# Performance work log

Measured on AMD Instinct MI355X. Metric: run time of the kernel, lower is better.

## Reference

```python
import jax, jax.numpy as jnp
import numpy as np

B, C, H, W = 8, 384, 32, 32
NH, DK, DV = 8, 48, 48
CFF = 4 * C
L = H * W
NBIAS = (2 * H - 1) * (2 * W - 1)
LN_EPS = 1e-5


def _relative_indices(height, width):
    # rel_idx[q, k] = (gy_k - gy_q + H) * W + (gx_k - gx_q + W), matching the torch loop
    gy, gx = np.meshgrid(np.arange(height), np.arange(width), indexing='ij')
    gy = gy.ravel(); gx = gx.ravel()
    rel = (gy[None, :] - gy[:, None] + height) * width + (gx[None, :] - gx[:, None] + width)
    return jnp.asarray(rel, dtype=jnp.int64)


def setup_inputs() -> dict:
    key = jax.random.key(0)
    ks = jax.random.split(key, 10)
    s = 0.02  # small init scale
    return {
        'x': jax.random.normal(ks[0], (B, C, H, W), dtype=jnp.float32),
        'gamma': jnp.ones((C,), jnp.float32),
        'beta': jnp.zeros((C,), jnp.float32),
        'Wq': jax.random.normal(ks[1], (NH * DK, C), jnp.float32) * s,
        'Wk': jax.random.normal(ks[2], (NH * DK, C), jnp.float32) * s,
        'Wv': jax.random.normal(ks[3], (NH * DV, C), jnp.float32) * s,
        'Wo': jax.random.normal(ks[4], (C, NH * DV), jnp.float32) * s,
        'bo': jnp.zeros((C,), jnp.float32),
        'rel_bias': jax.random.normal(ks[5], (NH, NBIAS), jnp.float32),
        'fc1_w': jax.random.normal(ks[6], (CFF, C), jnp.float32) * s,
        'fc1_b': jnp.zeros((CFF,), jnp.float32),
        'fc2_w': jax.random.normal(ks[7], (C, CFF), jnp.float32) * s,
        'fc2_b': jnp.zeros((C,), jnp.float32),
        'rel_idx': _relative_indices(H, W),
    }


def reference(x, gamma, beta, Wq, Wk, Wv, Wo, bo, rel_bias,
              fc1_w, fc1_b, fc2_w, fc2_b, rel_idx):
    b, c, h_sp, w_sp = x.shape
    l = h_sp * w_sp
    nh = rel_bias.shape[0]
    dk = Wq.shape[0] // nh
    dv = Wv.shape[0] // nh

    # LayerNorm over channel dim (NHWC), then flatten to tokens [b, l, c]
    t = jnp.transpose(x, (0, 2, 3, 1))
    mu = jnp.mean(t, axis=-1, keepdims=True)
    var = jnp.mean(jnp.square(t - mu), axis=-1, keepdims=True)
    t = (t - mu) / jnp.sqrt(var + LN_EPS) * gamma + beta
    tok = t.reshape(b, l, c)

    q = (tok @ Wq.T).reshape(b, l, nh, dk)
    k = (tok @ Wk.T).reshape(b, l, nh, dk)
    v = (tok @ Wv.T).reshape(b, l, nh, dv)

    # gathered relative position bias: [nh, l, l]
    bias = rel_bias[:, rel_idx]
    # note: original applies NO 1/sqrt(d_k) scaling
    scores = jnp.einsum('blhd,bmhd->bhlm', q, k) + bias[None]
    attn = jax.nn.softmax(scores, axis=-1)
    out = jnp.einsum('bhlm,bmhd->blhd', attn, v).reshape(b, l, nh * dv)
    out = out @ Wo.T + bo  # [b, l, c]
    out = jnp.transpose(out, (0, 2, 1)).reshape(b, c, h_sp, w_sp)

    y = x + out  # attention residual (x_stem = x, no downsampling)

    # FFN: 1x1 convs == per-pixel linear over channels; exact (erf) gelu as torch default
    u = jnp.einsum('bchw,oc->bohw', y, fc1_w) + fc1_b[None, :, None, None]
    u = jax.nn.gelu(u, approximate=False)
    u = jnp.einsum('bchw,oc->bohw', u, fc2_w) + fc2_b[None, :, None, None]
    return y + u
```

## Files before the change

### kernel.cpp

```cpp
#include <hip/hip_runtime.h>
#include <math.h>

#define SL 1024
#define CH 384
#define NHEAD 8
#define DH 48
#define NBIAS 3969
#define NTOK 8192
#define BATCH 8
#define CFF 1536
#define LN_EPS 1e-5f
#define QKVLD 1152

#define WQKV_OFF 0
#define WO_OFF   442368
#define F1_OFF   589824
#define F2_OFF   1179648
#define WTOT     1769472

typedef float floatx4 __attribute__((ext_vector_type(4)));
typedef short bf16x8 __attribute__((ext_vector_type(8)));

__device__ __forceinline__ unsigned f2bf_u(float f) {
  unsigned u = __float_as_uint(f);
  return (u + 0x7fffu + ((u >> 16) & 1u)) >> 16;
}
__device__ __forceinline__ unsigned pack2(float a, float b) {
  return f2bf_u(a) | (f2bf_u(b) << 16);
}

__device__ __forceinline__ void gload_lds16(const void* g, void* l) {
  __builtin_amdgcn_global_load_lds(
      (const __attribute__((address_space(1))) void*)g,
      (__attribute__((address_space(3))) void*)l, 16, 0, 0);
}

__global__ void k_transpose_in(const float* __restrict__ x, float* __restrict__ xt) {
  __shared__ float s[32][33];
  int b = blockIdx.z;
  int c0 = blockIdx.y * 32, l0 = blockIdx.x * 32;
  int tx = threadIdx.x, ty = threadIdx.y;
  const float* xb = x + (size_t)b * CH * SL;
  float* xtb = xt + (size_t)b * SL * CH;
#pragma unroll
  for (int i = 0; i < 4; i++) {
    int c = c0 + ty * 4 + i;
    s[ty * 4 + i][tx] = xb[(size_t)c * SL + l0 + tx];
  }
  __syncthreads();
#pragma unroll
  for (int i = 0; i < 4; i++) {
    int l = l0 + ty * 4 + i;
    xtb[(size_t)l * CH + c0 + tx] = s[tx][ty * 4 + i];
  }
}

__global__ void k_transpose_add_out(const float* __restrict__ y, const float* __restrict__ u,
                                    float* __restrict__ out) {
  __shared__ float s[32][33];
  int b = blockIdx.z;
  int c0 = blockIdx.y * 32, l0 = blockIdx.x * 32;
  int tx = threadIdx.x, ty = threadIdx.y;
  const float* yb = y + (size_t)b * SL * CH;
  const float* ub = u + (size_t)b * SL * CH;
  float* ob = out + (size_t)b * CH * SL;
#pragma unroll
  for (int i = 0; i < 4; i++) {
    int l = l0 + ty * 4 + i;
    size_t idx = (size_t)l * CH + c0 + tx;
    s[ty * 4 + i][tx] = yb[idx] + ub[idx];
  }
  __syncthreads();
#pragma unroll
  for (int i = 0; i < 4; i++) {
    int c = c0 + ty * 4 + i;
    ob[(size_t)c * SL + l0 + tx] = s[tx][ty * 4 + i];
  }
}

__global__ void k_w2bf(const float* __restrict__ Wq, const float* __restrict__ Wk,
                       const float* __restrict__ Wv, const float* __restrict__ Wo,
                       const float* __restrict__ f1, const float* __restrict__ f2,
                       short* __restrict__ dst) {
  size_t i = ((size_t)blockIdx.x * 256 + threadIdx.x) * 8;
  if (i >= WTOT) return;
  const float* s;
  size_t base;
  if (i < 147456)        { s = Wq; base = 0; }
  else if (i < 294912)   { s = Wk; base = 147456; }
  else if (i < WO_OFF)   { s = Wv; base = 294912; }
  else if (i < F1_OFF)   { s = Wo; base = WO_OFF; }
  else if (i < F2_OFF)   { s = f1; base = F1_OFF; }
  else                   { s = f2; base = F2_OFF; }
  const float4* p = (const float4*)(s + (i - base));
  float4 a = p[0], b = p[1];
  uint4 o;
  o.x = pack2(a.x, a.y); o.y = pack2(a.z, a.w);
  o.z = pack2(b.x, b.y); o.w = pack2(b.z, b.w);
  *(uint4*)(dst + i) = o;
}

__global__ void k_layernorm(const float* __restrict__ xt, const float* __restrict__ gamma,
                            const float* __restrict__ beta, short* __restrict__ tok) {
  int t = blockIdx.x;
  const float* row = xt + (size_t)t * CH;
  short* orow = tok + (size_t)t * CH;
  int tid = threadIdx.x;
  float v0 = row[tid], v1 = row[tid + 128], v2 = row[tid + 256];
  float s = v0 + v1 + v2;
  float q = v0 * v0 + v1 * v1 + v2 * v2;
#pragma unroll
  for (int mask = 32; mask; mask >>= 1) {
    s += __shfl_xor(s, mask, 64);
    q += __shfl_xor(q, mask, 64);
  }
  __shared__ float sh[4];
  if ((tid & 63) == 0) {
    sh[(tid >> 6) * 2] = s;
    sh[(tid >> 6) * 2 + 1] = q;
  }
  __syncthreads();
  s = sh[0] + sh[2];
  q = sh[1] + sh[3];
  float mu = s * (1.0f / CH);
  float var = q * (1.0f / CH) - mu * mu;
  float rstd = rsqrtf(var + LN_EPS);
  orow[tid]       = (short)f2bf_u((v0 - mu) * rstd * gamma[tid] + beta[tid]);
  orow[tid + 128] = (short)f2bf_u((v1 - mu) * rstd * gamma[tid + 128] + beta[tid + 128]);
  orow[tid + 256] = (short)f2bf_u((v2 - mu) * rstd * gamma[tid + 256] + beta[tid + 256]);
}

template <int BM, bool GELU, bool HAS_BIAS, bool HAS_RES, bool OUT_F32, bool OUT_BF>
__global__ __launch_bounds__(256) void k_gemm_mfma(
    const short* __restrict__ A, const short* __restrict__ W,
    const float* __restrict__ bias, const float* __restrict__ res,
    float* __restrict__ Cf, short* __restrict__ Cb, int N, int K) {
  constexpr int MI = BM / 32;
  constexpr int ASI = BM * 2 / 64;
  __shared__ short As[BM * 64];
  __shared__ short Bs[128 * 64];
  int tid = threadIdx.x;
  int wid = tid >> 6, lane = tid & 63;
  int lanelo = lane & 15, quad = lane >> 4;
  int wm = wid & 1, wn = wid >> 1;
  int m0 = blockIdx.y * BM, n0 = blockIdx.x * 128;

  const short* Aga[ASI];
  short* Ala[ASI];
#pragma unroll
  for (int s = 0; s < ASI; s++) {
    int p = wid * (BM * 2) + s * 64 + lane;
    int row = p >> 3, ch = (p & 7) ^ (row & 7);
    Aga[s] = A + (size_t)(m0 + row) * K + ch * 8;
    Ala[s] = As + (wid * (BM * 2) + s * 64) * 8;
  }
  const short* Bga[4];
  short* Bla[4];
#pragma unroll
  for (int s = 0; s < 4; s++) {
    int p = wid * 256 + s * 64 + lane;
    int row = p >> 3, ch = (p & 7) ^ (row & 7);
    Bga[s] = W + (size_t)(n0 + row) * K + ch * 8;
    Bla[s] = Bs + (wid * 256 + s * 64) * 8;
  }

  floatx4 acc[MI][4];
#pragma unroll
  for (int i = 0; i < MI; i++)
#pragma unroll
    for (int j = 0; j < 4; j++) acc[i][j] = {0.f, 0.f, 0.f, 0.f};

  int x8 = lanelo & 7;
  int ca0 = (quad ^ x8) * 8;
  int ca1 = ((quad + 4) ^ x8) * 8;

  for (int k0 = 0; k0 < K; k0 += 64) {
    __syncthreads();
#pragma unroll
    for (int s = 0; s < ASI; s++) gload_lds16(Aga[s] + k0, Ala[s]);
#pragma unroll
    for (int s = 0; s < 4; s++) gload_lds16(Bga[s] + k0, Bla[s]);
    __syncthreads();
#pragma unroll
    for (int h = 0; h < 2; h++) {
      int co = h ? ca1 : ca0;
      bf16x8 af[MI], bq[4];
#pragma unroll
      for (int i = 0; i < MI; i++)
        af[i] = *(const bf16x8*)&As[(wm * (BM / 2) + i * 16 + lanelo) * 64 + co];
#pragma unroll
      for (int j = 0; j < 4; j++)
        bq[j] = *(const bf16x8*)&Bs[(wn * 64 + j * 16 + lanelo) * 64 + co];
#pragma unroll
      for (int i = 0; i < MI; i++)
#pragma unroll
        for (int j = 0; j < 4; j++)
          acc[i][j] = __builtin_amdgcn_mfma_f32_16x16x32_bf16(af[i], bq[j], acc[i][j], 0, 0, 0);
    }
  }

  int colb = n0 + wn * 64 + lanelo;
  float bvv[4];
#pragma unroll
  for (int j = 0; j < 4; j++) bvv[j] = HAS_BIAS ? bias[colb + j * 16] : 0.0f;
#pragma unroll
  for (int i = 0; i < MI; i++) {
    int r = m0 + wm * (BM / 2) + i * 16 + quad * 4;
#pragma unroll
    for (int j = 0; j < 4; j++) {
      int c = colb + j * 16;
#pragma unroll
      for (int reg = 0; reg < 4; reg++) {
        float v = acc[i][j][reg] + bvv[j];
        size_t idx = (size_t)(r + reg) * N + c;
        if (HAS_RES) v += res[idx];
        if (GELU) v = 0.5f * v * (1.0f + erff(v * 0.7071067811865476f));
        if (OUT_F32) Cf[idx] = v;
        if (OUT_BF) Cb[idx] = (short)f2bf_u(v);
      }
    }
  }
}

__global__ __launch_bounds__(256) void k_attn_mfma(
    const short* __restrict__ qkv, const float* __restrict__ rel_bias,
    short* __restrict__ ao) {
  __shared__ short Qs[64 * 72];
  __shared__ short Ks[64 * 72];
  __shared__ short Vts[48 * 72];
  __shared__ short Ps[4 * 16 * 72];

  int b = blockIdx.z, h = blockIdx.y;
  int l0 = blockIdx.x * 64;
  int tid = threadIdx.x;
  int wid = tid >> 6, lane = tid & 63;
  int lanelo = lane & 15, quad = lane >> 4;
  size_t bSL = (size_t)b * SL;
  const float* rbh = rel_bias + h * NBIAS;

  int srow = tid / 3, spos = tid - srow * 3;
  int vmp = tid & 31, vdg = tid >> 5;

  if (tid < 192) {
    const short* src = qkv + (bSL + l0 + srow) * QKVLD + h * DH;
    *(uint4*)&Qs[srow * 72 + spos * 8]      = *(const uint4*)(src + spos * 8);
    *(uint4*)&Qs[srow * 72 + 24 + spos * 8] = *(const uint4*)(src + 24 + spos * 8);
  }
  for (int z = tid; z < 64 * 8; z += 256) {
    int r = z >> 3, u = z & 7;
    ((unsigned*)&Qs[r * 72 + 48])[u] = 0u;
    ((unsigned*)&Ks[r * 72 + 48])[u] = 0u;
  }
  __syncthreads();

  bf16x8 aq0 = *(const bf16x8*)&Qs[(wid * 16 + lanelo) * 72 + quad * 8];
  bf16x8 aq1 = *(const bf16x8*)&Qs[(wid * 16 + lanelo) * 72 + 32 + quad * 8];

  floatx4 O0 = {0.f, 0.f, 0.f, 0.f}, O1 = O0, O2 = O0;
  float lsum[4] = {0.f, 0.f, 0.f, 0.f};

  const float* rb[4];
  {
    int lq = l0 + wid * 16 + quad * 4;
#pragma unroll
    for (int reg = 0; reg < 4; reg++) {
      int l = lq + reg;
      rb[reg] = rbh + (1056 - (l >> 5) * 32 - (l & 31)) + lanelo;
    }
  }

  short* Pw = &Ps[wid * 16 * 72];

  for (int mt = 0; mt < SL; mt += 64) {
    __syncthreads();
    if (tid < 192) {
      {
        const short* src = qkv + (bSL + mt + srow) * QKVLD + 384 + h * DH;
        *(uint4*)&Ks[srow * 72 + spos * 8]      = *(const uint4*)(src + spos * 8);
        *(uint4*)&Ks[srow * 72 + 24 + spos * 8] = *(const uint4*)(src + 24 + spos * 8);
      }
      {
        const short* vs0 = qkv + (bSL + mt + 2 * vmp) * QKVLD + 768 + h * DH + vdg * 8;
        union { uint4 u; unsigned short s[8]; } va, vb;
        va.u = *(const uint4*)vs0;
        vb.u = *(const uint4*)(vs0 + QKVLD);
#pragma unroll
        for (int i = 0; i < 8; i++) {
          unsigned pk = (unsigned)va.s[i] | ((unsigned)vb.s[i] << 16);
          *(unsigned*)&Vts[(vdg * 8 + i) * 72 + 2 * vmp] = pk;
        }
      }
    }
    __syncthreads();

    floatx4 sarr[4];
#pragma unroll
    for (int nt = 0; nt < 4; nt++) {
      floatx4 acc = {0.f, 0.f, 0.f, 0.f};
      bf16x8 b0 = *(const bf16x8*)&Ks[(nt * 16 + lanelo) * 72 + quad * 8];
      bf16x8 b1 = *(const bf16x8*)&Ks[(nt * 16 + lanelo) * 72 + 32 + quad * 8];
      acc = __builtin_amdgcn_mfma_f32_16x16x32_bf16(aq0, b0, acc, 0, 0, 0);
      acc = __builtin_amdgcn_mfma_f32_16x16x32_bf16(aq1, b1, acc, 0, 0, 0);
      sarr[nt] = acc;
    }

#pragma unroll
    for (int nt = 0; nt < 4; nt++) {
      int mo = mt + nt * 16;
#pragma unroll
      for (int reg = 0; reg < 4; reg++) {
        float e = __expf(sarr[nt][reg] + rb[reg][mo]);
        lsum[reg] += e;
        Pw[(quad * 4 + reg) * 72 + nt * 16 + lanelo] = (short)f2bf_u(e);
      }
    }
    __asm__ volatile("s_waitcnt lgkmcnt(0)" ::: "memory");
    bf16x8 pa0 = *(const bf16x8*)&Pw[lanelo * 72 + quad * 8];
    bf16x8 pa1 = *(const bf16x8*)&Pw[lanelo * 72 + 32 + quad * 8];

    {
      bf16x8 vb0 = *(const bf16x8*)&Vts[(0 * 16 + lanelo) * 72 + quad * 8];
      bf16x8 vb1 = *(const bf16x8*)&Vts[(0 * 16 + lanelo) * 72 + 32 + quad * 8];
      O0 = __builtin_amdgcn_mfma_f32_16x16x32_bf16(pa0, vb0, O0, 0, 0, 0);
      O0 = __builtin_amdgcn_mfma_f32_16x16x32_bf16(pa1, vb1, O0, 0, 0, 0);
    }
    {
      bf16x8 vb0 = *(const bf16x8*)&Vts[(1 * 16 + lanelo) * 72 + quad * 8];
      bf16x8 vb1 = *(const bf16x8*)&Vts[(1 * 16 + lanelo) * 72 + 32 + quad * 8];
      O1 = __builtin_amdgcn_mfma_f32_16x16x32_bf16(pa0, vb0, O1, 0, 0, 0);
      O1 = __builtin_amdgcn_mfma_f32_16x16x32_bf16(pa1, vb1, O1, 0, 0, 0);
    }
    {
      bf16x8 vb0 = *(const bf16x8*)&Vts[(2 * 16 + lanelo) * 72 + quad * 8];
      bf16x8 vb1 = *(const bf16x8*)&Vts[(2 * 16 + lanelo) * 72 + 32 + quad * 8];
      O2 = __builtin_amdgcn_mfma_f32_16x16x32_bf16(pa0, vb0, O2, 0, 0, 0);
      O2 = __builtin_amdgcn_mfma_f32_16x16x32_bf16(pa1, vb1, O2, 0, 0, 0);
    }
  }

#pragma unroll
  for (int reg = 0; reg < 4; reg++) {
    float s = lsum[reg];
    s += __shfl_xor(s, 1, 64);
    s += __shfl_xor(s, 2, 64);
    s += __shfl_xor(s, 4, 64);
    s += __shfl_xor(s, 8, 64);
    float inv = 1.0f / s;
    size_t base = (bSL + (size_t)(l0 + wid * 16 + quad * 4 + reg)) * CH + h * DH;
    ao[base + 0 + lanelo]  = (short)f2bf_u(O0[reg] * inv);
    ao[base + 16 + lanelo] = (short)f2bf_u(O1[reg] * inv);
    ao[base + 32 + lanelo] = (short)f2bf_u(O2[reg] * inv);
  }
}

extern "C" void kernel_launch(void* const* d_in, const int* in_sizes, int n_in,
                              void* d_out, int out_size, void* d_ws, size_t ws_size,
                              hipStream_t stream) {
  const float* x = (const float*)d_in[0];
  const float* gamma = (const float*)d_in[1];
  const float* beta = (const float*)d_in[2];
  const float* Wq = (const float*)d_in[3];
  const float* Wk = (const float*)d_in[4];
  const float* Wv = (const float*)d_in[5];
  const float* Wo = (const float*)d_in[6];
  const float* bo = (const float*)d_in[7];
  const float* rel_bias = (const float*)d_in[8];
  const float* fc1_w = (const float*)d_in[9];
  const float* fc1_b = (const float*)d_in[10];
  const float* fc2_w = (const float*)d_in[11];
  const float* fc2_b = (const float*)d_in[12];
  float* out = (float*)d_out;

  const size_t TOKCH = (size_t)NTOK * CH;
  float* ws_f = (float*)d_ws;
  float* xt = ws_f;
  float* yb = xt + TOKCH;
  float* ub = yb + TOKCH;
  short* sbase = (short*)(ub + TOKCH);
  short* wbf    = sbase;
  short* tok_bf = wbf + WTOT;
  short* qkv_bf = tok_bf + TOKCH;
  short* ao_bf  = qkv_bf + (size_t)NTOK * QKVLD;
  short* yb_bf  = ao_bf + TOKCH;
  short* h1_bf  = yb_bf + TOKCH;

  dim3 tgrid(SL / 32, CH / 32, BATCH);
  dim3 tblk(32, 8);
  k_transpose_in<<<tgrid, tblk, 0, stream>>>(x, xt);
  k_w2bf<<<WTOT / 8 / 256, 256, 0, stream>>>(Wq, Wk, Wv, Wo, fc1_w, fc2_w, wbf);
  k_layernorm<<<NTOK, 128, 0, stream>>>(xt, gamma, beta, tok_bf);

  k_gemm_mfma<128, false, false, false, false, true>
      <<<dim3(QKVLD / 128, NTOK / 128), 256, 0, stream>>>(
          tok_bf, wbf + WQKV_OFF, nullptr, nullptr, nullptr, qkv_bf, QKVLD, CH);

  k_attn_mfma<<<dim3(SL / 64, NHEAD, BATCH), 256, 0, stream>>>(qkv_bf, rel_bias, ao_bf);

  k_gemm_mfma<64, false, true, true, true, true>
      <<<dim3(CH / 128, NTOK / 64), 256, 0, stream>>>(
          ao_bf, wbf + WO_OFF, bo, xt, yb, yb_bf, CH, CH);

  k_gemm_mfma<128, true, true, false, false, true>
      <<<dim3(CFF / 128, NTOK / 128), 256, 0, stream>>>(
          yb_bf, wbf + F1_OFF, fc1_b, nullptr, nullptr, h1_bf, CFF, CH);

  k_gemm_mfma<64, false, true, false, true, false>
      <<<dim3(CH / 128, NTOK / 64), 256, 0, stream>>>(
          h1_bf, wbf + F2_OFF, fc2_b, nullptr, ub, nullptr, CH, CFF);

  k_transpose_add_out<<<tgrid, tblk, 0, stream>>>(yb, ub, out);
}
```

Measured before the change: 229.5 us.

## Fuse input/output transposes into LayerNorm and GEMM epilogues; widen attention tile

The input NCHW-to-token transpose is folded into a new LayerNorm kernel that stages a 32-token by 384-channel tile in LDS. The Wo GEMM now reads its residual straight from NCHW x, and the fc2 GEMM adds the yb residual and writes NCHW output directly, which removes two transpose kernels and the xt and ub intermediates. Attention now handles 128 query rows per block with two 16-row sub-tiles per wave, reusing each K/V LDS load for twice as many rows, and the P buffer shares space with Q. The trade-offs are strided float4 stores of the output in the GEMM epilogue and higher register and LDS use per block in attention and LayerNorm.

```diff
diff --git a/kernel.cpp b/kernel.cpp
--- a/kernel.cpp
+++ b/kernel.cpp
@@ -33,49 +33,6 @@
   __builtin_amdgcn_global_load_lds(
       (const __attribute__((address_space(1))) void*)g,
       (__attribute__((address_space(3))) void*)l, 16, 0, 0);
-}
-
-__global__ void k_transpose_in(const float* __restrict__ x, float* __restrict__ xt) {
-  __shared__ float s[32][33];
-  int b = blockIdx.z;
-  int c0 = blockIdx.y * 32, l0 = blockIdx.x * 32;
-  int tx = threadIdx.x, ty = threadIdx.y;
-  const float* xb = x + (size_t)b * CH * SL;
-  float* xtb = xt + (size_t)b * SL * CH;
-#pragma unroll
-  for (int i = 0; i < 4; i++) {
-    int c = c0 + ty * 4 + i;
-    s[ty * 4 + i][tx] = xb[(size_t)c * SL + l0 + tx];
-  }
-  __syncthreads();
-#pragma unroll
-  for (int i = 0; i < 4; i++) {
-    int l = l0 + ty * 4 + i;
-    xtb[(size_t)l * CH + c0 + tx] = s[tx][ty * 4 + i];
-  }
-}
-
-__global__ void k_transpose_add_out(const float* __restrict__ y, const float* __restrict__ u,
-                                    float* __restrict__ out) {
-  __shared__ float s[32][33];
-  int b = blockIdx.z;
-  int c0 = blockIdx.y * 32, l0 = blockIdx.x * 32;
-  int tx = threadIdx.x, ty = threadIdx.y;
-  const float* yb = y + (size_t)b * SL * CH;
-  const float* ub = u + (size_t)b * SL * CH;
-  float* ob = out + (size_t)b * CH * SL;
-#pragma unroll
-  for (int i = 0; i < 4; i++) {
-    int l = l0 + ty * 4 + i;
-    size_t idx = (size_t)l * CH + c0 + tx;
-    s[ty * 4 + i][tx] = yb[idx] + ub[idx];
-  }
-  __syncthreads();
-#pragma unroll
-  for (int i = 0; i < 4; i++) {
-    int c = c0 + ty * 4 + i;
-    ob[(size_t)c * SL + l0 + tx] = s[tx][ty * 4 + i];
-  }
 }
 
 __global__ void k_w2bf(const float* __restrict__ Wq, const float* __restrict__ Wk,
@@ -100,41 +57,50 @@
   *(uint4*)(dst + i) = o;
 }
 
-__global__ void k_layernorm(const float* __restrict__ xt, const float* __restrict__ gamma,
-                            const float* __restrict__ beta, short* __restrict__ tok) {
-  int t = blockIdx.x;
-  const float* row = xt + (size_t)t * CH;
-  short* orow = tok + (size_t)t * CH;
+__global__ __launch_bounds__(256) void k_ln_fused(
+    const float* __restrict__ x, const float* __restrict__ gamma,
+    const float* __restrict__ beta, short* __restrict__ tok) {
+  __shared__ float sx[32][385];
+  int b = blockIdx.y, l0 = blockIdx.x * 32;
   int tid = threadIdx.x;
-  float v0 = row[tid], v1 = row[tid + 128], v2 = row[tid + 256];
-  float s = v0 + v1 + v2;
-  float q = v0 * v0 + v1 * v1 + v2 * v2;
-#pragma unroll
-  for (int mask = 32; mask; mask >>= 1) {
-    s += __shfl_xor(s, mask, 64);
-    q += __shfl_xor(q, mask, 64);
-  }
-  __shared__ float sh[4];
-  if ((tid & 63) == 0) {
-    sh[(tid >> 6) * 2] = s;
-    sh[(tid >> 6) * 2 + 1] = q;
+  const float* xb = x + (size_t)b * CH * SL;
+  int cr = tid >> 3, ls = (tid & 7) * 4;
+#pragma unroll
+  for (int c0 = 0; c0 < CH; c0 += 32) {
+    int c = c0 + cr;
+    float4 v = *(const float4*)(xb + (size_t)c * SL + l0 + ls);
+    sx[ls + 0][c] = v.x; sx[ls + 1][c] = v.y;
+    sx[ls + 2][c] = v.z; sx[ls + 3][c] = v.w;
   }
   __syncthreads();
-  s = sh[0] + sh[2];
-  q = sh[1] + sh[3];
+  int tl = tid >> 3, p = tid & 7;
+  float vals[48];
+  float s = 0.f, q = 0.f;
+#pragma unroll
+  for (int i = 0; i < 48; i++) {
+    float v = sx[tl][p * 48 + i];
+    vals[i] = v; s += v; q += v * v;
+  }
+  s += __shfl_xor(s, 1, 64); q += __shfl_xor(q, 1, 64);
+  s += __shfl_xor(s, 2, 64); q += __shfl_xor(q, 2, 64);
+  s += __shfl_xor(s, 4, 64); q += __shfl_xor(q, 4, 64);
   float mu = s * (1.0f / CH);
-  float var = q * (1.0f / CH) - mu * mu;
-  float rstd = rsqrtf(var + LN_EPS);
-  orow[tid]       = (short)f2bf_u((v0 - mu) * rstd * gamma[tid] + beta[tid]);
-  orow[tid + 128] = (short)f2bf_u((v1 - mu) * rstd * gamma[tid + 128] + beta[tid + 128]);
-  orow[tid + 256] = (short)f2bf_u((v2 - mu) * rstd * gamma[tid + 256] + beta[tid + 256]);
-}
-
-template <int BM, bool GELU, bool HAS_BIAS, bool HAS_RES, bool OUT_F32, bool OUT_BF>
+  float rstd = rsqrtf(q * (1.0f / CH) - mu * mu + LN_EPS);
+  short* orow = tok + (size_t)(b * SL + l0 + tl) * CH + p * 48;
+#pragma unroll
+  for (int i = 0; i < 48; i += 2) {
+    float a = (vals[i] - mu) * rstd * gamma[p * 48 + i] + beta[p * 48 + i];
+    float c = (vals[i + 1] - mu) * rstd * gamma[p * 48 + i + 1] + beta[p * 48 + i + 1];
+    *(unsigned*)(orow + i) = pack2(a, c);
+  }
+}
+
+template <int BM, bool GELU, bool HAS_BIAS, int RES_MODE, int OUT_MODE>
 __global__ __launch_bounds__(256) void k_gemm_mfma(
     const short* __restrict__ A, const short* __restrict__ W,
     const float* __restrict__ bias, const float* __restrict__ res,
-    float* __restrict__ Cf, short* __restrict__ Cb, int N, int K) {
+    float* __restrict__ Cf, short* __restrict__ Cb, float* __restrict__ Ct,
+    int N, int K) {
   constexpr int MI = BM / 32;
   constexpr int ASI = BM * 2 / 64;
   __shared__ short As[BM * 64];
@@ -206,17 +172,32 @@
 #pragma unroll
   for (int i = 0; i < MI; i++) {
     int r = m0 + wm * (BM / 2) + i * 16 + quad * 4;
+    int bb = r >> 10, ll = r & 1023;
 #pragma unroll
     for (int j = 0; j < 4; j++) {
       int c = colb + j * 16;
+      float4 rv = {0.f, 0.f, 0.f, 0.f};
+      if (RES_MODE == 2) rv = *(const float4*)(res + ((size_t)bb * CH + c) * SL + ll);
+      float vv[4];
 #pragma unroll
       for (int reg = 0; reg < 4; reg++) {
         float v = acc[i][j][reg] + bvv[j];
-        size_t idx = (size_t)(r + reg) * N + c;
-        if (HAS_RES) v += res[idx];
+        if (RES_MODE == 1) v += res[(size_t)(r + reg) * N + c];
+        if (RES_MODE == 2) v += (&rv.x)[reg];
         if (GELU) v = 0.5f * v * (1.0f + erff(v * 0.7071067811865476f));
-        if (OUT_F32) Cf[idx] = v;
-        if (OUT_BF) Cb[idx] = (short)f2bf_u(v);
+        vv[reg] = v;
+      }
+      if (OUT_MODE & 1) {
+#pragma unroll
+        for (int reg = 0; reg < 4; reg++) Cf[(size_t)(r + reg) * N + c] = vv[reg];
+      }
+      if (OUT_MODE & 2) {
+#pragma unroll
+        for (int reg = 0; reg < 4; reg++) Cb[(size_t)(r + reg) * N + c] = (short)f2bf_u(vv[reg]);
+      }
+      if (OUT_MODE & 4) {
+        float4 ov = {vv[0], vv[1], vv[2], vv[3]};
+        *(float4*)(Ct + ((size_t)bb * CH + c) * SL + ll) = ov;
       }
     }
   }
@@ -225,13 +206,12 @@
 __global__ __launch_bounds__(256) void k_attn_mfma(
     const short* __restrict__ qkv, const float* __restrict__ rel_bias,
     short* __restrict__ ao) {
-  __shared__ short Qs[64 * 72];
+  __shared__ short QP[128 * 72];
   __shared__ short Ks[64 * 72];
   __shared__ short Vts[48 * 72];
-  __shared__ short Ps[4 * 16 * 72];
 
   int b = blockIdx.z, h = blockIdx.y;
-  int l0 = blockIdx.x * 64;
+  int l0 = blockIdx.x * 128;
   int tid = threadIdx.x;
   int wid = tid >> 6, lane = tid & 63;
   int lanelo = lane & 15, quad = lane >> 4;
@@ -241,35 +221,37 @@
   int srow = tid / 3, spos = tid - srow * 3;
   int vmp = tid & 31, vdg = tid >> 5;
 
-  if (tid < 192) {
-    const short* src = qkv + (bSL + l0 + srow) * QKVLD + h * DH;
-    *(uint4*)&Qs[srow * 72 + spos * 8]      = *(const uint4*)(src + spos * 8);
-    *(uint4*)&Qs[srow * 72 + 24 + spos * 8] = *(const uint4*)(src + 24 + spos * 8);
-  }
-  for (int z = tid; z < 64 * 8; z += 256) {
+  for (int g = tid; g < 768; g += 256) {
+    int row = g / 6, pos = g - row * 6;
+    *(uint4*)&QP[row * 72 + pos * 8] =
+        *(const uint4*)(qkv + (bSL + l0 + row) * QKVLD + h * DH + pos * 8);
+  }
+  for (int z = tid; z < 128 * 8; z += 256) {
     int r = z >> 3, u = z & 7;
-    ((unsigned*)&Qs[r * 72 + 48])[u] = 0u;
-    ((unsigned*)&Ks[r * 72 + 48])[u] = 0u;
+    ((unsigned*)&QP[r * 72 + 48])[u] = 0u;
+    if (r < 64) ((unsigned*)&Ks[r * 72 + 48])[u] = 0u;
   }
   __syncthreads();
 
-  bf16x8 aq0 = *(const bf16x8*)&Qs[(wid * 16 + lanelo) * 72 + quad * 8];
-  bf16x8 aq1 = *(const bf16x8*)&Qs[(wid * 16 + lanelo) * 72 + 32 + quad * 8];
-
-  floatx4 O0 = {0.f, 0.f, 0.f, 0.f}, O1 = O0, O2 = O0;
-  float lsum[4] = {0.f, 0.f, 0.f, 0.f};
-
-  const float* rb[4];
-  {
-    int lq = l0 + wid * 16 + quad * 4;
-#pragma unroll
-    for (int reg = 0; reg < 4; reg++) {
-      int l = lq + reg;
-      rb[reg] = rbh + (1056 - (l >> 5) * 32 - (l & 31)) + lanelo;
-    }
-  }
-
-  short* Pw = &Ps[wid * 16 * 72];
+  bf16x8 aq[2][2];
+#pragma unroll
+  for (int i = 0; i < 2; i++) {
+    aq[i][0] = *(const bf16x8*)&QP[(wid * 32 + i * 16 + lanelo) * 72 + quad * 8];
+    aq[i][1] = *(const bf16x8*)&QP[(wid * 32 + i * 16 + lanelo) * 72 + 32 + quad * 8];
+  }
+
+  floatx4 O[2][3];
+#pragma unroll
+  for (int i = 0; i < 2; i++)
+#pragma unroll
+    for (int d = 0; d < 3; d++) O[i][d] = {0.f, 0.f, 0.f, 0.f};
+  float lsum[2][4] = {{0.f, 0.f, 0.f, 0.f}, {0.f, 0.f, 0.f, 0.f}};
+  int boff[2];
+#pragma unroll
+  for (int i = 0; i < 2; i++)
+    boff[i] = 1056 - (l0 + wid * 32 + i * 16 + quad * 4) + lanelo;
+
+  short* Pw = &QP[wid * 32 * 72];
 
   for (int mt = 0; mt < SL; mt += 64) {
     __syncthreads();
@@ -293,64 +275,69 @@
     }
     __syncthreads();
 
-    floatx4 sarr[4];
+    bf16x8 kb[4][2];
 #pragma unroll
     for (int nt = 0; nt < 4; nt++) {
-      floatx4 acc = {0.f, 0.f, 0.f, 0.f};
-      bf16x8 b0 = *(const bf16x8*)&Ks[(nt * 16 + lanelo) * 72 + quad * 8];
-      bf16x8 b1 = *(const bf16x8*)&Ks[(nt * 16 + lanelo) * 72 + 32 + quad * 8];
-      acc = __builtin_amdgcn_mfma_f32_16x16x32_bf16(aq0, b0, acc, 0, 0, 0);
-      acc = __builtin_amdgcn_mfma_f32_16x16x32_bf16(aq1, b1, acc, 0, 0, 0);
-      sarr[nt] = acc;
-    }
-
-#pragma unroll
-    for (int nt = 0; nt < 4; nt++) {
-      int mo = mt + nt * 16;
-#pragma unroll
-      for (int reg = 0; reg < 4; reg++) {
-        float e = __expf(sarr[nt][reg] + rb[reg][mo]);
-        lsum[reg] += e;
-        Pw[(quad * 4 + reg) * 72 + nt * 16 + lanelo] = (short)f2bf_u(e);
+      kb[nt][0] = *(const bf16x8*)&Ks[(nt * 16 + lanelo) * 72 + quad * 8];
+      kb[nt][1] = *(const bf16x8*)&Ks[(nt * 16 + lanelo) * 72 + 32 + quad * 8];
+    }
+
+#pragma unroll
+    for (int i = 0; i < 2; i++) {
+      floatx4 s[4];
+#pragma unroll
+      for (int nt = 0; nt < 4; nt++) {
+        floatx4 a = {0.f, 0.f, 0.f, 0.f};
+        a = __builtin_amdgcn_mfma_f32_16x16x32_bf16(aq[i][0], kb[nt][0], a, 0, 0, 0);
+        a = __builtin_amdgcn_mfma_f32_16x16x32_bf16(aq[i][1], kb[nt][1], a, 0, 0, 0);
+        s[nt] = a;
+      }
+#pragma unroll
+      for (int nt = 0; nt < 4; nt++) {
+        int mo = mt + nt * 16;
+#pragma unroll
+        for (int reg = 0; reg < 4; reg++) {
+          float e = __expf(s[nt][reg] + rbh[boff[i] - reg + mo]);
+          lsum[i][reg] += e;
+          Pw[(i * 16 + quad * 4 + reg) * 72 + nt * 16 + lanelo] = (short)f2bf_u(e);
+        }
       }
     }
     __asm__ volatile("s_waitcnt lgkmcnt(0)" ::: "memory");
-    bf16x8 pa0 = *(const bf16x8*)&Pw[lanelo * 72 + quad * 8];
-    bf16x8 pa1 = *(const bf16x8*)&Pw[lanelo * 72 + 32 + quad * 8];
-
-    {
-      bf16x8 vb0 = *(const bf16x8*)&Vts[(0 * 16 + lanelo) * 72 + quad * 8];
-      bf16x8 vb1 = *(const bf16x8*)&Vts[(0 * 16 + lanelo) * 72 + 32 + quad * 8];
-      O0 = __builtin_amdgcn_mfma_f32_16x16x32_bf16(pa0, vb0, O0, 0, 0, 0);
-      O0 = __builtin_amdgcn_mfma_f32_16x16x32_bf16(pa1, vb1, O0, 0, 0, 0);
-    }
-    {
-      bf16x8 vb0 = *(const bf16x8*)&Vts[(1 * 16 + lanelo) * 72 + quad * 8];
-      bf16x8 vb1 = *(const bf16x8*)&Vts[(1 * 16 + lanelo) * 72 + 32 + quad * 8];
-      O1 = __builtin_amdgcn_mfma_f32_16x16x32_bf16(pa0, vb0, O1, 0, 0, 0);
-      O1 = __builtin_amdgcn_mfma_f32_16x16x32_bf16(pa1, vb1, O1, 0, 0, 0);
-    }
-    {
-      bf16x8 vb0 = *(const bf16x8*)&Vts[(2 * 16 + lanelo) * 72 + quad * 8];
-      bf16x8 vb1 = *(const bf16x8*)&Vts[(2 * 16 + lanelo) * 72 + 32 + quad * 8];
-      O2 = __builtin_amdgcn_mfma_f32_16x16x32_bf16(pa0, vb0, O2, 0, 0, 0);
-      O2 = __builtin_amdgcn_mfma_f32_16x16x32_bf16(pa1, vb1, O2, 0, 0, 0);
-    }
-  }
-
-#pragma unroll
-  for (int reg = 0; reg < 4; reg++) {
-    float s = lsum[reg];
-    s += __shfl_xor(s, 1, 64);
-    s += __shfl_xor(s, 2, 64);
-    s += __shfl_xor(s, 4, 64);
-    s += __shfl_xor(s, 8, 64);
-    float inv = 1.0f / s;
-    size_t base = (bSL + (size_t)(l0 + wid * 16 + quad * 4 + reg)) * CH + h * DH;
-    ao[base + 0 + lanelo]  = (short)f2bf_u(O0[reg] * inv);
-    ao[base + 16 + lanelo] = (short)f2bf_u(O1[reg] * inv);
-    ao[base + 32 + lanelo] = (short)f2bf_u(O2[reg] * inv);
-  }
+    bf16x8 pa[2][2];
+#pragma unroll
+    for (int i = 0; i < 2; i++) {
+      pa[i][0] = *(const bf16x8*)&Pw[(i * 16 + lanelo) * 72 + quad * 8];
+      pa[i][1] = *(const bf16x8*)&Pw[(i * 16 + lanelo) * 72 + 32 + quad * 8];
+    }
+#pragma unroll
+    for (int d = 0; d < 3; d++) {
+      bf16x8 v0 = *(const bf16x8*)&Vts[(d * 16 + lanelo) * 72 + quad * 8];
+      bf16x8 v1 = *(const bf16x8*)&Vts[(d * 16 + lanelo) * 72 + 32 + quad * 8];
+#pragma unroll
+      for (int i = 0; i < 2; i++) {
+        O[i][d] = __builtin_amdgcn_mfma_f32_16x16x32_bf16(pa[i][0], v0, O[i][d], 0, 0, 0);
+        O[i][d] = __builtin_amdgcn_mfma_f32_16x16x32_bf16(pa[i][1], v1, O[i][d], 0, 0, 0);
+      }
+    }
+  }
+
+#pragma unroll
+  for (int i = 0; i < 2; i++)
+#pragma unroll
+    for (int reg = 0; reg < 4; reg++) {
+      float s = lsum[i][reg];
+      s += __shfl_xor(s, 1, 64);
+      s += __shfl_xor(s, 2, 64);
+      s += __shfl_xor(s, 4, 64);
+      s += __shfl_xor(s, 8, 64);
+      float inv = 1.0f / s;
+      size_t base =
+          (bSL + (size_t)(l0 + wid * 32 + i * 16 + quad * 4 + reg)) * CH + h * DH;
+      ao[base + 0 + lanelo]  = (short)f2bf_u(O[i][0][reg] * inv);
+      ao[base + 16 + lanelo] = (short)f2bf_u(O[i][1][reg] * inv);
+      ao[base + 32 + lanelo] = (short)f2bf_u(O[i][2][reg] * inv);
+    }
 }
 
 extern "C" void kernel_launch(void* const* d_in, const int* in_sizes, int n_in,
@@ -373,40 +360,33 @@
 
   const size_t TOKCH = (size_t)NTOK * CH;
   float* ws_f = (float*)d_ws;
-  float* xt = ws_f;
-  float* yb = xt + TOKCH;
-  float* ub = yb + TOKCH;
-  short* sbase = (short*)(ub + TOKCH);
-  short* wbf    = sbase;
+  float* yb = ws_f;
+  short* wbf    = (short*)(yb + TOKCH);
   short* tok_bf = wbf + WTOT;
   short* qkv_bf = tok_bf + TOKCH;
   short* ao_bf  = qkv_bf + (size_t)NTOK * QKVLD;
   short* yb_bf  = ao_bf + TOKCH;
   short* h1_bf  = yb_bf + TOKCH;
 
-  dim3 tgrid(SL / 32, CH / 32, BATCH);
-  dim3 tblk(32, 8);
-  k_transpose_in<<<tgrid, tblk, 0, stream>>>(x, xt);
   k_w2bf<<<WTOT / 8 / 256, 256, 0, stream>>>(Wq, Wk, Wv, Wo, fc1_w, fc2_w, wbf);
-  k_layernorm<<<NTOK, 128, 0, stream>>>(xt, gamma, beta, tok_bf);
-
-  k_gemm_mfma<128, false, false, false, false, true>
+  k_ln_fused<<<dim3(SL / 32, BATCH), 256, 0, stream>>>(x, gamma, beta, tok_bf);
+
+  k_gemm_mfma<128, false, false, 0, 2>
       <<<dim3(QKVLD / 128, NTOK / 128), 256, 0, stream>>>(
-          tok_bf, wbf + WQKV_OFF, nullptr, nullptr, nullptr, qkv_bf, QKVLD, CH);
-
-  k_attn_mfma<<<dim3(SL / 64, NHEAD, BATCH), 256, 0, stream>>>(qkv_bf, rel_bias, ao_bf);
-
-  k_gemm_mfma<64, false, true, true, true, true>
+          tok_bf, wbf + WQKV_OFF, nullptr, nullptr, nullptr, qkv_bf, nullptr,
+          QKVLD, CH);
+
+  k_attn_mfma<<<dim3(SL / 128, NHEAD, BATCH), 256, 0, stream>>>(qkv_bf, rel_bias, ao_bf);
+
+  k_gemm_mfma<64, false, true, 2, 3>
       <<<dim3(CH / 128, NTOK / 64), 256, 0, stream>>>(
-          ao_bf, wbf + WO_OFF, bo, xt, yb, yb_bf, CH, CH);
-
-  k_gemm_mfma<128, true, true, false, false, true>
+          ao_bf, wbf + WO_OFF, bo, x, yb, yb_bf, nullptr, CH, CH);
+
+  k_gemm_mfma<128, true, true, 0, 2>
       <<<dim3(CFF / 128, NTOK / 128), 256, 0, stream>>>(
-          yb_bf, wbf + F1_OFF, fc1_b, nullptr, nullptr, h1_bf, CFF, CH);
-
-  k_gemm_mfma<64, false, true, false, true, false>
+          yb_bf, wbf + F1_OFF, fc1_b, nullptr, nullptr, h1_bf, nullptr, CFF, CH);
+
+  k_gemm_mfma<64, false, true, 1, 4>
       <<<dim3(CH / 128, NTOK / 64), 256, 0, stream>>>(
-          h1_bf, wbf + F2_OFF, fc2_b, nullptr, ub, nullptr, CH, CFF);
-
-  k_transpose_add_out<<<tgrid, tblk, 0, stream>>>(yb, ub, out);
-}
+          h1_bf, wbf + F2_OFF, fc2_b, yb, nullptr, nullptr, out, CH, CFF);
+}
```

Result: faster. 218.5 us (-4.8%).
